# Kernel optimization log

Hardware: AMD Instinct MI355X
Metric: run time of the kernel (lower is better)

## Reference

```python
import jax, jax.numpy as jnp
import numpy as np

B, T, D, H = 4, 2048, 1152, 8
HD = D // H          # 144
ROT = HD             # full rotary
SCALE = HD ** -0.5


def _rotate_half(x):
    # x: [..., ROT]
    x1, x2 = x[..., : ROT // 2], x[..., ROT // 2 :]
    return jnp.concatenate([-x2, x1], axis=-1)


def _apply_rotary(q, k, cos, sin):
    # q,k: [B,H,T,HD]; cos,sin: [T,ROT] broadcast over B,H
    q_rot, q_pass = q[..., :ROT], q[..., ROT:]
    k_rot, k_pass = k[..., :ROT], k[..., ROT:]
    q = jnp.concatenate([q_rot * cos + _rotate_half(q_rot) * sin, q_pass], axis=-1)
    k = jnp.concatenate([k_rot * cos + _rotate_half(k_rot) * sin, k_pass], axis=-1)
    return q, k


def setup_inputs() -> dict:
    key = jax.random.key(0)
    ks = jax.random.split(key, 7)
    init = 1.0 / np.sqrt(D)  # keep activations well-scaled
    return {
        "x": jax.random.normal(ks[0], (B, T, D), dtype=jnp.float32),
        "cos": jax.random.uniform(ks[1], (T, ROT), dtype=jnp.float32),
        "sin": jax.random.uniform(ks[2], (T, ROT), dtype=jnp.float32),
        "Wq": jax.random.normal(ks[3], (D, D), dtype=jnp.float32) * init,
        "Wk": jax.random.normal(ks[4], (D, D), dtype=jnp.float32) * init,
        "Wv": jax.random.normal(ks[5], (D, D), dtype=jnp.float32) * init,
        "Wo": jax.random.normal(ks[6], (D, D), dtype=jnp.float32) * init,
    }


def reference(x, cos, sin, Wq, Wk, Wv, Wo):
    # nn.Linear(bias=False): y = x @ W.T
    def proj(W):
        y = jnp.einsum("btd,ed->bte", x, W)
        return y.reshape(B, T, H, HD).transpose(0, 2, 1, 3)  # [B,H,T,HD]

    q, k, v = proj(Wq), proj(Wk), proj(Wv)
    q, k = _apply_rotary(q, k, cos, sin)
    scores = jnp.einsum("bhqd,bhkd->bhqk", q, k) * SCALE
    attn = jax.nn.softmax(scores, axis=-1)
    o = jnp.einsum("bhqk,bhkd->bhqd", attn, v)
    o = o.transpose(0, 2, 1, 3).reshape(B, T, D)
    return jnp.einsum("btd,ed->bte", o, Wo)
```

## Files before the change

kernel.cpp:

```cpp
#include <hip/hip_runtime.h>
#include <cstdint>
#include <cstddef>

typedef __bf16 bf16;
typedef bf16 bf16x8 __attribute__((ext_vector_type(8)));
typedef bf16 bf16x4 __attribute__((ext_vector_type(4)));
typedef bf16 bf16x2 __attribute__((ext_vector_type(2)));
typedef float f32x4 __attribute__((ext_vector_type(4)));
typedef float f32x16 __attribute__((ext_vector_type(16)));
typedef uint32_t u32x2 __attribute__((ext_vector_type(2)));
typedef uint32_t u32x4 __attribute__((ext_vector_type(4)));

#define DEVI __device__ __forceinline__

#define CB 4
#define CT 2048
#define CD 1152
#define CH 8
#define CHD 144
#define CBT 8192
#define LOG2E 1.44269504f

DEVI void gload_lds16(const void* g, void* l) {
  __builtin_amdgcn_global_load_lds(
      (const __attribute__((address_space(1))) void*)g,
      (__attribute__((address_space(3))) void*)l, 16, 0, 0);
}

DEVI f32x4 mfma16(bf16x8 a, bf16x8 b, f32x4 c) {
  return __builtin_amdgcn_mfma_f32_16x16x32_bf16(a, b, c, 0, 0, 0);
}
DEVI f32x16 mfma32(bf16x8 a, bf16x8 b, f32x16 c) {
  return __builtin_amdgcn_mfma_f32_32x32x16_bf16(a, b, c, 0, 0, 0);
}

DEVI uint32_t cvtpk(float lo, float hi) {
  uint32_t r;
  asm("v_cvt_pk_bf16_f32 %0, %1, %2" : "=v"(r) : "v"(lo), "v"(hi));
  return r;
}

DEVI f32x16 zero16() {
  f32x16 z;
#pragma unroll
  for (int i = 0; i < 16; ++i) z[i] = 0.f;
  return z;
}

__global__ __launch_bounds__(256) void k_cast(const float* __restrict__ in,
                                              bf16* __restrict__ out, int n8) {
  int i = blockIdx.x * 256 + threadIdx.x;
  if (i >= n8) return;
  const float4* p = (const float4*)in + (size_t)i * 2;
  float4 a = p[0], b = p[1];
  bf16x8 o;
  o[0] = (bf16)a.x; o[1] = (bf16)a.y; o[2] = (bf16)a.z; o[3] = (bf16)a.w;
  o[4] = (bf16)b.x; o[5] = (bf16)b.y; o[6] = (bf16)b.z; o[7] = (bf16)b.w;
  ((bf16x8*)out)[i] = o;
}

__global__ __launch_bounds__(256) void k_cast4(
    const float* __restrict__ a, const float* __restrict__ b,
    const float* __restrict__ c, const float* __restrict__ d,
    bf16* __restrict__ oa, bf16* __restrict__ ob,
    bf16* __restrict__ oc, bf16* __restrict__ od, int n8) {
  int w = blockIdx.y;
  const float* in = (w == 0) ? a : (w == 1) ? b : (w == 2) ? c : d;
  bf16* out = (w == 0) ? oa : (w == 1) ? ob : (w == 2) ? oc : od;
  int i = blockIdx.x * 256 + threadIdx.x;
  if (i >= n8) return;
  const float4* p = (const float4*)in + (size_t)i * 2;
  float4 x = p[0], y = p[1];
  bf16x8 o;
  o[0] = (bf16)x.x; o[1] = (bf16)x.y; o[2] = (bf16)x.z; o[3] = (bf16)x.w;
  o[4] = (bf16)y.x; o[5] = (bf16)y.y; o[6] = (bf16)y.z; o[7] = (bf16)y.w;
  ((bf16x8*)out)[i] = o;
}

template <bool BF16_OUT>
DEVI void gemm_body(const bf16* __restrict__ A, const bf16* __restrict__ W,
                    void* __restrict__ Cout, int M, int N, int K,
                    int bm0, int bn0) {
  __shared__ __align__(16) bf16 As[128 * 40];
  __shared__ __align__(16) bf16 Bs[128 * 40];
  const int tid = threadIdx.x;
  const int lane = tid & 63, wid = tid >> 6;
  const int l15 = lane & 15, g = lane >> 4;
  const int wm = wid >> 1, wn = wid & 1;

  f32x4 acc[4][4];
  for (int mi = 0; mi < 4; ++mi)
    for (int ni = 0; ni < 4; ++ni) {
      acc[mi][ni][0] = 0.f; acc[mi][ni][1] = 0.f;
      acc[mi][ni][2] = 0.f; acc[mi][ni][3] = 0.f;
    }

  const int nk = K >> 5;
  for (int kt = 0; kt < nk; ++kt) {
    const int k0 = kt << 5;
    for (int c = 0; c < 3; ++c) {
      int li = tid + (c << 8);
      if (li < 640) {
        int e0 = li << 3;
        int row = e0 / 40, col = e0 % 40;
        if (col >= 32) col = 24;
        gload_lds16(&A[(size_t)(bm0 + row) * K + k0 + col], As + (size_t)(li & ~63) * 8);
        gload_lds16(&W[(size_t)(bn0 + row) * K + k0 + col], Bs + (size_t)(li & ~63) * 8);
      }
    }
    __syncthreads();

    bf16x8 af[4], bfr[4];
    for (int mi = 0; mi < 4; ++mi)
      af[mi] = *(const bf16x8*)&As[(wm * 64 + mi * 16 + l15) * 40 + g * 8];
    for (int ni = 0; ni < 4; ++ni)
      bfr[ni] = *(const bf16x8*)&Bs[(wn * 64 + ni * 16 + l15) * 40 + g * 8];
    __builtin_amdgcn_s_setprio(1);
    for (int mi = 0; mi < 4; ++mi)
      for (int ni = 0; ni < 4; ++ni)
        acc[mi][ni] = mfma16(af[mi], bfr[ni], acc[mi][ni]);
    __builtin_amdgcn_s_setprio(0);
    __syncthreads();
  }

  for (int mi = 0; mi < 4; ++mi)
    for (int ni = 0; ni < 4; ++ni)
      for (int r = 0; r < 4; ++r) {
        int rowg = bm0 + wm * 64 + mi * 16 + g * 4 + r;
        int colg = bn0 + wn * 64 + ni * 16 + l15;
        float v = acc[mi][ni][r];
        if (BF16_OUT)
          ((bf16*)Cout)[(size_t)rowg * N + colg] = (bf16)v;
        else
          ((float*)Cout)[(size_t)rowg * N + colg] = v;
      }
}

__global__ __launch_bounds__(256) void k_gemm_qkv(
    const bf16* __restrict__ A, const bf16* __restrict__ Wq,
    const bf16* __restrict__ Wk, const bf16* __restrict__ Wv,
    bf16* __restrict__ q, bf16* __restrict__ k, bf16* __restrict__ v) {
  const int nx = gridDim.x, ny = gridDim.y;
  const int nwg = nx * ny * gridDim.z;
  const int orig = (blockIdx.z * ny + blockIdx.y) * nx + blockIdx.x;
  const int logical = (orig & 7) * (nwg >> 3) + (orig >> 3);
  const int lx = logical % nx;
  const int rest = logical / nx;
  const int ly = rest % ny, lz = rest / ny;
  const bf16* W = (lz == 0) ? Wq : (lz == 1) ? Wk : Wv;
  bf16* out = (lz == 0) ? q : (lz == 1) ? k : v;
  gemm_body<true>(A, W, out, CBT, CD, CD, ly * 128, lx * 128);
}

__global__ __launch_bounds__(256) void k_gemm_out(
    const bf16* __restrict__ A, const bf16* __restrict__ W, float* __restrict__ out) {
  const int nx = gridDim.x, ny = gridDim.y;
  const int nwg = nx * ny;
  const int orig = blockIdx.y * nx + blockIdx.x;
  const int logical = (orig & 7) * (nwg >> 3) + (orig >> 3);
  const int lx = logical % nx, ly = logical / nx;
  gemm_body<false>(A, W, out, CBT, CD, CD, ly * 128, lx * 128);
}

__global__ __launch_bounds__(256) void k_rotary(bf16* __restrict__ q, bf16* __restrict__ k,
                                                const float* __restrict__ cosb,
                                                const float* __restrict__ sinb) {
  const int bt = blockIdx.x;
  const int t = bt & (CT - 1);
  const size_t rowoff = (size_t)bt * CD;
  const float* cr = cosb + (size_t)t * CHD;
  const float* sr = sinb + (size_t)t * CHD;
  for (int i = threadIdx.x; i < 288; i += 256) {
    int tensor = i / 144;
    int rem = i - tensor * 144;
    int h = rem / 18, jg = rem % 18;
    int j = jg * 4;
    float scl = tensor ? 1.0f : 0.08333333333f;
    bf16* base = (tensor ? k : q) + rowoff + h * CHD;
    bf16x4 a = *(bf16x4*)&base[j];
    bf16x4 b2 = *(bf16x4*)&base[j + 72];
    f32x4 c1 = *(const f32x4*)&cr[j];
    f32x4 s1 = *(const f32x4*)&sr[j];
    f32x4 c2 = *(const f32x4*)&cr[j + 72];
    f32x4 s2 = *(const f32x4*)&sr[j + 72];
    bf16x4 o1, o2;
    for (int r = 0; r < 4; ++r) {
      float av = (float)a[r], bv = (float)b2[r];
      o1[r] = (bf16)((av * c1[r] - bv * s1[r]) * scl);
      o2[r] = (bf16)((bv * c2[r] + av * s2[r]) * scl);
    }
    *(bf16x4*)&base[j] = o1;
    *(bf16x4*)&base[j + 72] = o2;
  }
}

__global__ __launch_bounds__(256) void k_vtrans(const bf16* __restrict__ v, bf16* __restrict__ vT) {
  __shared__ bf16 tile[64][152];
  const int bh = blockIdx.y;
  const int b = bh >> 3, h = bh & 7;
  const int t0 = blockIdx.x * 64;
  for (int i8 = threadIdx.x; i8 < 64 * 18; i8 += 256) {
    int r = i8 / 18, c8 = i8 % 18;
    *(bf16x8*)&tile[r][c8 * 8] =
        *(const bf16x8*)&v[((size_t)(b * CT + t0 + r)) * CD + h * CHD + c8 * 8];
  }
  __syncthreads();
  for (int o = threadIdx.x; o < CHD * 64; o += 256) {
    int hd = o / 64, j = o & 63;
    vT[((size_t)(bh * CHD + hd)) * CT + t0 + j] = tile[j][hd];
  }
}

DEVI void build_pfrag(const f32x16& s, float m, float& ps, bf16x8& f0, bf16x8& f1) {
  uint32_t pk[8];
#pragma unroll
  for (int a = 0; a < 8; ++a) {
    float p0 = exp2f((s[2 * a] - m) * LOG2E);
    float p1 = exp2f((s[2 * a + 1] - m) * LOG2E);
    ps += p0 + p1;
    pk[a] = cvtpk(p0, p1);
  }
  u32x2 r02 = __builtin_amdgcn_permlane32_swap(pk[0], pk[2], false, false);
  u32x2 r13 = __builtin_amdgcn_permlane32_swap(pk[1], pk[3], false, false);
  u32x2 r46 = __builtin_amdgcn_permlane32_swap(pk[4], pk[6], false, false);
  u32x2 r57 = __builtin_amdgcn_permlane32_swap(pk[5], pk[7], false, false);
  u32x4 w0 = {r02[0], r13[0], r02[1], r13[1]};
  u32x4 w1 = {r46[0], r57[0], r46[1], r57[1]};
  f0 = __builtin_bit_cast(bf16x8, w0);
  f1 = __builtin_bit_cast(bf16x8, w1);
}

__global__ __launch_bounds__(512, 2) void k_attn(const bf16* __restrict__ qg,
                                                 const bf16* __restrict__ kg,
                                                 const bf16* __restrict__ vT,
                                                 bf16* __restrict__ og) {
  const int lin = blockIdx.x;
  const int xcd = lin & 7, idx = lin >> 3;
  const int bh = ((idx & 3) << 3) | xcd;
  const int qx = idx >> 2;
  const int b = bh >> 3, h = bh & 7;
  const int q0 = qx << 8;
  const int tid = threadIdx.x, lane = tid & 63, wq = tid >> 6;
  const int l31 = lane & 31, hi = lane >> 5;
  const int hi16 = hi * 16;
  const int kxor = (l31 & 7) << 4;

  constexpr int KBUF = 64 * 192;
  constexpr int VBUF = 160 * 64;
  __shared__ __align__(16) bf16 Ks[2 * KBUF];
  __shared__ __align__(16) bf16 Vs[2 * VBUF];

  bf16x8 qf[9];
  {
    const bf16* qbase = qg + (size_t)(b * CT + q0 + wq * 32 + l31) * CD + h * CHD + hi * 8;
#pragma unroll
    for (int ks = 0; ks < 9; ++ks) qf[ks] = *(const bf16x8*)&qbase[ks * 16];
  }

  const bf16* ksrc[3];
  const bf16* vsrc[3];
  int kldo[3], vldo[3];
#pragma unroll
  for (int it = 0; it < 3; ++it) {
    int c = tid + it * 512;
    int krow = c / 24, kj = c - krow * 24;
    int kcol = (kj * 16) ^ ((krow & 7) << 4);
    if (kcol >= 288) kcol = 0;
    ksrc[it] = kg + (size_t)(b * CT + krow) * CD + h * CHD + (kcol >> 1);
    kldo[it] = ((tid & ~63) + it * 512) * 8;
    int vr = c >> 3, vj = c & 7;
    int vcol = (vj * 16) ^ ((vr & 7) << 4);
    if (vr > 143) vr = 143;
    vsrc[it] = vT + (size_t)(bh * CHD + vr) * CT + (vcol >> 1);
    vldo[it] = ((tid & ~63) + it * 512) * 8;
  }
  const bool vok2 = (tid < 128);

  if (tid < 256) {
    u32x4 z = {0u, 0u, 0u, 0u};
    int bsel = tid >> 7, off = tid & 127;
    *(u32x4*)(Vs + bsel * VBUF + 144 * 64 + off * 8) = z;
  }

  {
    bf16* Kc = Ks;
    bf16* Vc = Vs;
#pragma unroll
    for (int it = 0; it < 3; ++it) gload_lds16(ksrc[it], Kc + kldo[it]);
#pragma unroll
    for (int it = 0; it < 2; ++it) gload_lds16(vsrc[it], Vc + vldo[it]);
    if (vok2) gload_lds16(vsrc[2], Vc + vldo[2]);
  }
  __syncthreads();

  f32x16 oacc[5];
#pragma unroll
  for (int t = 0; t < 5; ++t) oacc[t] = zero16();
  float mrow = -__builtin_inff();
  float lsum = 0.f;

  int cur = 0;
  for (int t = 0; t < 32; ++t) {
    bf16* Kc = Ks + cur * KBUF;
    bf16* Vc = Vs + cur * VBUF;

    if (t < 31) {
      bf16* Kn = Ks + (cur ^ 1) * KBUF;
      bf16* Vn = Vs + (cur ^ 1) * VBUF;
      const int kvn = (t + 1) << 6;
#pragma unroll
      for (int it = 0; it < 3; ++it) gload_lds16(ksrc[it] + (size_t)kvn * CD, Kn + kldo[it]);
#pragma unroll
      for (int it = 0; it < 2; ++it) gload_lds16(vsrc[it] + kvn, Vn + vldo[it]);
      if (vok2) gload_lds16(vsrc[2] + kvn, Vn + vldo[2]);
    }
    __builtin_amdgcn_sched_barrier(0);

    const char* kr0 = (const char*)Kc + (size_t)l31 * 384;
    const char* kr1 = kr0 + 32 * 384;
    f32x16 s0 = zero16(), s1 = zero16();
    __builtin_amdgcn_s_setprio(1);
#pragma unroll
    for (int ks = 0; ks < 9; ++ks) {
      int off = (ks * 32 + hi16) ^ kxor;
      s0 = mfma32(*(const bf16x8*)(kr0 + off), qf[ks], s0);
      s1 = mfma32(*(const bf16x8*)(kr1 + off), qf[ks], s1);
    }
    __builtin_amdgcn_s_setprio(0);

    float mt = s0[0];
#pragma unroll
    for (int i = 1; i < 16; ++i) mt = fmaxf(mt, s0[i]);
#pragma unroll
    for (int i = 0; i < 16; ++i) mt = fmaxf(mt, s1[i]);
    mt = fmaxf(mt, __shfl_xor(mt, 32));

    if (mt > mrow + 5.5452f) {
      float alpha = exp2f((mrow - mt) * LOG2E);
      lsum *= alpha;
#pragma unroll
      for (int u = 0; u < 5; ++u) oacc[u] = oacc[u] * alpha;
      mrow = mt;
    }

    float ps = 0.f;
    bf16x8 pf0, pf1, pf2, pf3;
    build_pfrag(s0, mrow, ps, pf0, pf1);
    build_pfrag(s1, mrow, ps, pf2, pf3);
    ps += __shfl_xor(ps, 32);
    lsum += ps;

    __builtin_amdgcn_s_setprio(1);
#pragma unroll
    for (int u = 0; u < 5; ++u) {
      const char* vrow = (const char*)Vc + (size_t)(u * 32 + l31) * 128;
      oacc[u] = mfma32(*(const bf16x8*)(vrow + ((0 * 32 + hi16) ^ kxor)), pf0, oacc[u]);
      oacc[u] = mfma32(*(const bf16x8*)(vrow + ((1 * 32 + hi16) ^ kxor)), pf1, oacc[u]);
      oacc[u] = mfma32(*(const bf16x8*)(vrow + ((2 * 32 + hi16) ^ kxor)), pf2, oacc[u]);
      oacc[u] = mfma32(*(const bf16x8*)(vrow + ((3 * 32 + hi16) ^ kxor)), pf3, oacc[u]);
    }
    __builtin_amdgcn_s_setprio(0);

    __syncthreads();
    cur ^= 1;
  }

  float inv = 1.0f / lsum;
  bf16* ob = og + (size_t)(b * CT + q0 + wq * 32 + l31) * CD + h * CHD;
#pragma unroll
  for (int u = 0; u < 5; ++u) {
#pragma unroll
    for (int pr = 0; pr < 8; ++pr) {
      if (u == 4 && pr >= 4) continue;
      int hd = u * 32 + ((2 * pr) & 3) + 8 * (pr >> 1) + 4 * hi;
      bf16x2 w;
      w[0] = (bf16)(oacc[u][2 * pr] * inv);
      w[1] = (bf16)(oacc[u][2 * pr + 1] * inv);
      *(bf16x2*)&ob[hd] = w;
    }
  }
}

extern "C" void kernel_launch(void* const* d_in, const int* in_sizes, int n_in,
                              void* d_out, int out_size, void* d_ws, size_t ws_size,
                              hipStream_t stream) {
  const float* x = (const float*)d_in[0];
  const float* cosb = (const float*)d_in[1];
  const float* sinb = (const float*)d_in[2];
  const float* Wq = (const float*)d_in[3];
  const float* Wk = (const float*)d_in[4];
  const float* Wv = (const float*)d_in[5];
  const float* Wo = (const float*)d_in[6];

  char* ws = (char*)d_ws;
  bf16* xb   = (bf16*)(ws + 0);
  bf16* wqb  = (bf16*)(ws + 18874368);
  bf16* wkb  = (bf16*)(ws + 21528576);
  bf16* wvb  = (bf16*)(ws + 24182784);
  bf16* wob  = (bf16*)(ws + 26836992);
  bf16* qlin = (bf16*)(ws + 29491200);
  bf16* klin = (bf16*)(ws + 48365568);
  bf16* vlin = (bf16*)(ws + 67239936);
  bf16* vT   = (bf16*)(ws + 86114304);

  k_cast<<<4608, 256, 0, stream>>>(x, xb, CBT * CD / 8);
  k_cast4<<<dim3(648, 4), 256, 0, stream>>>(Wq, Wk, Wv, Wo, wqb, wkb, wvb, wob,
                                            CD * CD / 8);

  k_gemm_qkv<<<dim3(CD / 128, CBT / 128, 3), 256, 0, stream>>>(xb, wqb, wkb, wvb,
                                                               qlin, klin, vlin);
  k_rotary<<<CB * CT, 256, 0, stream>>>(qlin, klin, cosb, sinb);
  k_vtrans<<<dim3(CT / 64, CB * CH), 256, 0, stream>>>(vlin, vT);
  k_attn<<<256, 512, 0, stream>>>(qlin, klin, vT, xb);
  k_gemm_out<<<dim3(CD / 128, CBT / 128), 256, 0, stream>>>(xb, wob, (float*)d_out);
}
```

Baseline: 275.9 us.

## Software-pipeline attention: overlap next QK^T with current softmax and PV

Restructures the attention loop so the QK^T scores for tile t are computed while tile t-1's softmax and PV MMAs run. V gets a triple-buffered LDS ring to match the lagged consumption. The log2(e) factor is folded into the Q pre-scale in the rotary kernel, which drops a multiply per exponent. The rescale threshold is raised and the row max uses a tree reduction. This costs more LDS and registers (two sets of score accumulators), which may limit occupancy at 2 blocks per CU.

```diff
diff --git a/kernel.cpp b/kernel.cpp
--- a/kernel.cpp
+++ b/kernel.cpp
@@ -19,7 +19,6 @@
 #define CH 8
 #define CHD 144
 #define CBT 8192
-#define LOG2E 1.44269504f
 
 DEVI void gload_lds16(const void* g, void* l) {
   __builtin_amdgcn_global_load_lds(
@@ -175,7 +174,7 @@
     int rem = i - tensor * 144;
     int h = rem / 18, jg = rem % 18;
     int j = jg * 4;
-    float scl = tensor ? 1.0f : 0.08333333333f;
+    float scl = tensor ? 1.0f : 0.120224587f;
     bf16* base = (tensor ? k : q) + rowoff + h * CHD;
     bf16x4 a = *(bf16x4*)&base[j];
     bf16x4 b2 = *(bf16x4*)&base[j + 72];
@@ -215,8 +214,8 @@
   uint32_t pk[8];
 #pragma unroll
   for (int a = 0; a < 8; ++a) {
-    float p0 = exp2f((s[2 * a] - m) * LOG2E);
-    float p1 = exp2f((s[2 * a + 1] - m) * LOG2E);
+    float p0 = exp2f(s[2 * a] - m);
+    float p1 = exp2f(s[2 * a + 1] - m);
     ps += p0 + p1;
     pk[a] = cvtpk(p0, p1);
   }
@@ -228,6 +227,19 @@
   u32x4 w1 = {r46[0], r57[0], r46[1], r57[1]};
   f0 = __builtin_bit_cast(bf16x8, w0);
   f1 = __builtin_bit_cast(bf16x8, w1);
+}
+
+DEVI float max32(const f32x16& s0, const f32x16& s1) {
+  float q0 = fmaxf(fmaxf(s0[0], s0[1]), fmaxf(s0[2], s0[3]));
+  float q1 = fmaxf(fmaxf(s0[4], s0[5]), fmaxf(s0[6], s0[7]));
+  float q2 = fmaxf(fmaxf(s0[8], s0[9]), fmaxf(s0[10], s0[11]));
+  float q3 = fmaxf(fmaxf(s0[12], s0[13]), fmaxf(s0[14], s0[15]));
+  float q4 = fmaxf(fmaxf(s1[0], s1[1]), fmaxf(s1[2], s1[3]));
+  float q5 = fmaxf(fmaxf(s1[4], s1[5]), fmaxf(s1[6], s1[7]));
+  float q6 = fmaxf(fmaxf(s1[8], s1[9]), fmaxf(s1[10], s1[11]));
+  float q7 = fmaxf(fmaxf(s1[12], s1[13]), fmaxf(s1[14], s1[15]));
+  return fmaxf(fmaxf(fmaxf(q0, q1), fmaxf(q2, q3)),
+               fmaxf(fmaxf(q4, q5), fmaxf(q6, q7)));
 }
 
 __global__ __launch_bounds__(512, 2) void k_attn(const bf16* __restrict__ qg,
@@ -248,7 +260,7 @@
   constexpr int KBUF = 64 * 192;
   constexpr int VBUF = 160 * 64;
   __shared__ __align__(16) bf16 Ks[2 * KBUF];
-  __shared__ __align__(16) bf16 Vs[2 * VBUF];
+  __shared__ __align__(16) bf16 Vs[3 * VBUF];
 
   bf16x8 qf[9];
   {
@@ -276,80 +288,77 @@
   }
   const bool vok2 = (tid < 128);
 
-  if (tid < 256) {
+  if (tid < 384) {
     u32x4 z = {0u, 0u, 0u, 0u};
     int bsel = tid >> 7, off = tid & 127;
     *(u32x4*)(Vs + bsel * VBUF + 144 * 64 + off * 8) = z;
   }
 
+#define STAGE_TILE(kv, kb, vb)                                              \
+  do {                                                                      \
+    bf16* Kn = Ks + (kb) * KBUF;                                            \
+    bf16* Vn = Vs + (vb) * VBUF;                                            \
+    _Pragma("unroll") for (int it = 0; it < 3; ++it)                        \
+        gload_lds16(ksrc[it] + (size_t)(kv) * CD, Kn + kldo[it]);           \
+    _Pragma("unroll") for (int it = 0; it < 2; ++it)                        \
+        gload_lds16(vsrc[it] + (kv), Vn + vldo[it]);                        \
+    if (vok2) gload_lds16(vsrc[2] + (kv), Vn + vldo[2]);                    \
+  } while (0)
+
+  STAGE_TILE(0, 0, 0);
+  __syncthreads();
+
+  f32x16 oacc[5];
+#pragma unroll
+  for (int u = 0; u < 5; ++u) oacc[u] = zero16();
+  float lsum = 0.f;
+  float m;
+  f32x16 sp0, sp1;
+
   {
-    bf16* Kc = Ks;
-    bf16* Vc = Vs;
-#pragma unroll
-    for (int it = 0; it < 3; ++it) gload_lds16(ksrc[it], Kc + kldo[it]);
-#pragma unroll
-    for (int it = 0; it < 2; ++it) gload_lds16(vsrc[it], Vc + vldo[it]);
-    if (vok2) gload_lds16(vsrc[2], Vc + vldo[2]);
-  }
-  __syncthreads();
-
-  f32x16 oacc[5];
-#pragma unroll
-  for (int t = 0; t < 5; ++t) oacc[t] = zero16();
-  float mrow = -__builtin_inff();
-  float lsum = 0.f;
-
-  int cur = 0;
-  for (int t = 0; t < 32; ++t) {
-    bf16* Kc = Ks + cur * KBUF;
-    bf16* Vc = Vs + cur * VBUF;
-
-    if (t < 31) {
-      bf16* Kn = Ks + (cur ^ 1) * KBUF;
-      bf16* Vn = Vs + (cur ^ 1) * VBUF;
-      const int kvn = (t + 1) << 6;
-#pragma unroll
-      for (int it = 0; it < 3; ++it) gload_lds16(ksrc[it] + (size_t)kvn * CD, Kn + kldo[it]);
-#pragma unroll
-      for (int it = 0; it < 2; ++it) gload_lds16(vsrc[it] + kvn, Vn + vldo[it]);
-      if (vok2) gload_lds16(vsrc[2] + kvn, Vn + vldo[2]);
-    }
+    STAGE_TILE(64, 1, 1);
     __builtin_amdgcn_sched_barrier(0);
-
-    const char* kr0 = (const char*)Kc + (size_t)l31 * 384;
+    const char* kr0 = (const char*)Ks + (size_t)l31 * 384;
     const char* kr1 = kr0 + 32 * 384;
-    f32x16 s0 = zero16(), s1 = zero16();
+    sp0 = zero16(); sp1 = zero16();
     __builtin_amdgcn_s_setprio(1);
 #pragma unroll
     for (int ks = 0; ks < 9; ++ks) {
       int off = (ks * 32 + hi16) ^ kxor;
-      s0 = mfma32(*(const bf16x8*)(kr0 + off), qf[ks], s0);
-      s1 = mfma32(*(const bf16x8*)(kr1 + off), qf[ks], s1);
+      sp0 = mfma32(*(const bf16x8*)(kr0 + off), qf[ks], sp0);
+      sp1 = mfma32(*(const bf16x8*)(kr1 + off), qf[ks], sp1);
     }
     __builtin_amdgcn_s_setprio(0);
-
-    float mt = s0[0];
-#pragma unroll
-    for (int i = 1; i < 16; ++i) mt = fmaxf(mt, s0[i]);
-#pragma unroll
-    for (int i = 0; i < 16; ++i) mt = fmaxf(mt, s1[i]);
+    float mt = max32(sp0, sp1);
     mt = fmaxf(mt, __shfl_xor(mt, 32));
-
-    if (mt > mrow + 5.5452f) {
-      float alpha = exp2f((mrow - mt) * LOG2E);
-      lsum *= alpha;
-#pragma unroll
-      for (int u = 0; u < 5; ++u) oacc[u] = oacc[u] * alpha;
-      mrow = mt;
-    }
+    m = mt;
+    __syncthreads();
+  }
+
+  for (int t = 1; t < 32; ++t) {
+    if (t < 31) STAGE_TILE((t + 1) << 6, (t + 1) & 1, (t + 1) % 3);
+    __builtin_amdgcn_sched_barrier(0);
+
+    const char* kr0 = (const char*)(Ks + (t & 1) * KBUF) + (size_t)l31 * 384;
+    const char* kr1 = kr0 + 32 * 384;
+    f32x16 sn0 = zero16(), sn1 = zero16();
+    __builtin_amdgcn_s_setprio(1);
+#pragma unroll
+    for (int ks = 0; ks < 9; ++ks) {
+      int off = (ks * 32 + hi16) ^ kxor;
+      sn0 = mfma32(*(const bf16x8*)(kr0 + off), qf[ks], sn0);
+      sn1 = mfma32(*(const bf16x8*)(kr1 + off), qf[ks], sn1);
+    }
+    __builtin_amdgcn_s_setprio(0);
 
     float ps = 0.f;
     bf16x8 pf0, pf1, pf2, pf3;
-    build_pfrag(s0, mrow, ps, pf0, pf1);
-    build_pfrag(s1, mrow, ps, pf2, pf3);
+    build_pfrag(sp0, m, ps, pf0, pf1);
+    build_pfrag(sp1, m, ps, pf2, pf3);
     ps += __shfl_xor(ps, 32);
     lsum += ps;
 
+    const bf16* Vc = Vs + ((t - 1) % 3) * VBUF;
     __builtin_amdgcn_s_setprio(1);
 #pragma unroll
     for (int u = 0; u < 5; ++u) {
@@ -361,9 +370,37 @@
     }
     __builtin_amdgcn_s_setprio(0);
 
+    float mt = max32(sn0, sn1);
+    mt = fmaxf(mt, __shfl_xor(mt, 32));
+    if (mt > m + 8.0f) {
+      float alpha = exp2f(m - mt);
+      lsum *= alpha;
+#pragma unroll
+      for (int u = 0; u < 5; ++u) oacc[u] = oacc[u] * alpha;
+      m = mt;
+    }
+    sp0 = sn0; sp1 = sn1;
     __syncthreads();
-    cur ^= 1;
-  }
+  }
+
+  {
+    float ps = 0.f;
+    bf16x8 pf0, pf1, pf2, pf3;
+    build_pfrag(sp0, m, ps, pf0, pf1);
+    build_pfrag(sp1, m, ps, pf2, pf3);
+    ps += __shfl_xor(ps, 32);
+    lsum += ps;
+    const bf16* Vc = Vs + (31 % 3) * VBUF;
+#pragma unroll
+    for (int u = 0; u < 5; ++u) {
+      const char* vrow = (const char*)Vc + (size_t)(u * 32 + l31) * 128;
+      oacc[u] = mfma32(*(const bf16x8*)(vrow + ((0 * 32 + hi16) ^ kxor)), pf0, oacc[u]);
+      oacc[u] = mfma32(*(const bf16x8*)(vrow + ((1 * 32 + hi16) ^ kxor)), pf1, oacc[u]);
+      oacc[u] = mfma32(*(const bf16x8*)(vrow + ((2 * 32 + hi16) ^ kxor)), pf2, oacc[u]);
+      oacc[u] = mfma32(*(const bf16x8*)(vrow + ((3 * 32 + hi16) ^ kxor)), pf3, oacc[u]);
+    }
+  }
+#undef STAGE_TILE
 
   float inv = 1.0f / lsum;
   bf16* ob = og + (size_t)(b * CT + q0 + wq * 32 + l31) * CD + h * CHD;
```

Result: slower. 281.8 us (+2.1%).

## Double-buffer GEMM LDS tiles and fold log2e into the Q scale

Applied to the files above, without the earlier changes.

The projection GEMM now keeps two LDS buffers per operand and issues the next K-slice's global-to-LDS loads before computing on the current slice. This hides load latency behind the MFMAs at the cost of twice the LDS. Separately, log2(e) is folded into the rotary Q scale so the softmax exp2 calls drop a multiply. The row-max reduction is rewritten as a tree, and the lazy-rescale threshold is retuned to the new base-2 units.

```diff
diff --git a/kernel.cpp b/kernel.cpp
--- a/kernel.cpp
+++ b/kernel.cpp
@@ -19,7 +19,6 @@
 #define CH 8
 #define CHD 144
 #define CBT 8192
-#define LOG2E 1.44269504f
 
 DEVI void gload_lds16(const void* g, void* l) {
   __builtin_amdgcn_global_load_lds(
@@ -81,12 +80,40 @@
 DEVI void gemm_body(const bf16* __restrict__ A, const bf16* __restrict__ W,
                     void* __restrict__ Cout, int M, int N, int K,
                     int bm0, int bn0) {
-  __shared__ __align__(16) bf16 As[128 * 40];
-  __shared__ __align__(16) bf16 Bs[128 * 40];
+  constexpr int TBUF = 128 * 40;
+  __shared__ __align__(16) bf16 As[2 * TBUF];
+  __shared__ __align__(16) bf16 Bs[2 * TBUF];
   const int tid = threadIdx.x;
   const int lane = tid & 63, wid = tid >> 6;
   const int l15 = lane & 15, g = lane >> 4;
   const int wm = wid >> 1, wn = wid & 1;
+
+  const bf16* asrc[3];
+  const bf16* wsrc[3];
+  int ldo[3];
+  bool on[3];
+#pragma unroll
+  for (int c = 0; c < 3; ++c) {
+    int li = tid + (c << 8);
+    on[c] = (li < 640);
+    int li2 = on[c] ? li : 0;
+    int e0 = li2 << 3;
+    int row = e0 / 40, col = e0 % 40;
+    if (col >= 32) col = 24;
+    asrc[c] = &A[(size_t)(bm0 + row) * K + col];
+    wsrc[c] = &W[(size_t)(bn0 + row) * K + col];
+    ldo[c] = (li2 & ~63) * 8;
+  }
+
+#define G_STAGE(k0, buf)                                                     \
+  do {                                                                       \
+    bf16* Ad = As + (buf)*TBUF;                                              \
+    bf16* Bd = Bs + (buf)*TBUF;                                              \
+    _Pragma("unroll") for (int c = 0; c < 3; ++c) if (on[c]) {               \
+      gload_lds16(asrc[c] + (k0), Ad + ldo[c]);                              \
+      gload_lds16(wsrc[c] + (k0), Bd + ldo[c]);                              \
+    }                                                                        \
+  } while (0)
 
   f32x4 acc[4][4];
   for (int mi = 0; mi < 4; ++mi)
@@ -96,32 +123,30 @@
     }
 
   const int nk = K >> 5;
+  G_STAGE(0, 0);
+  __syncthreads();
+
+  int cur = 0;
   for (int kt = 0; kt < nk; ++kt) {
-    const int k0 = kt << 5;
-    for (int c = 0; c < 3; ++c) {
-      int li = tid + (c << 8);
-      if (li < 640) {
-        int e0 = li << 3;
-        int row = e0 / 40, col = e0 % 40;
-        if (col >= 32) col = 24;
-        gload_lds16(&A[(size_t)(bm0 + row) * K + k0 + col], As + (size_t)(li & ~63) * 8);
-        gload_lds16(&W[(size_t)(bn0 + row) * K + k0 + col], Bs + (size_t)(li & ~63) * 8);
-      }
-    }
-    __syncthreads();
-
+    if (kt + 1 < nk) G_STAGE((kt + 1) << 5, cur ^ 1);
+    __builtin_amdgcn_sched_barrier(0);
+
+    const bf16* Ac = As + cur * TBUF;
+    const bf16* Bc = Bs + cur * TBUF;
     bf16x8 af[4], bfr[4];
     for (int mi = 0; mi < 4; ++mi)
-      af[mi] = *(const bf16x8*)&As[(wm * 64 + mi * 16 + l15) * 40 + g * 8];
+      af[mi] = *(const bf16x8*)&Ac[(wm * 64 + mi * 16 + l15) * 40 + g * 8];
     for (int ni = 0; ni < 4; ++ni)
-      bfr[ni] = *(const bf16x8*)&Bs[(wn * 64 + ni * 16 + l15) * 40 + g * 8];
+      bfr[ni] = *(const bf16x8*)&Bc[(wn * 64 + ni * 16 + l15) * 40 + g * 8];
     __builtin_amdgcn_s_setprio(1);
     for (int mi = 0; mi < 4; ++mi)
       for (int ni = 0; ni < 4; ++ni)
         acc[mi][ni] = mfma16(af[mi], bfr[ni], acc[mi][ni]);
     __builtin_amdgcn_s_setprio(0);
     __syncthreads();
-  }
+    cur ^= 1;
+  }
+#undef G_STAGE
 
   for (int mi = 0; mi < 4; ++mi)
     for (int ni = 0; ni < 4; ++ni)
@@ -175,7 +200,7 @@
     int rem = i - tensor * 144;
     int h = rem / 18, jg = rem % 18;
     int j = jg * 4;
-    float scl = tensor ? 1.0f : 0.08333333333f;
+    float scl = tensor ? 1.0f : 0.120224587f;
     bf16* base = (tensor ? k : q) + rowoff + h * CHD;
     bf16x4 a = *(bf16x4*)&base[j];
     bf16x4 b2 = *(bf16x4*)&base[j + 72];
@@ -215,8 +240,8 @@
   uint32_t pk[8];
 #pragma unroll
   for (int a = 0; a < 8; ++a) {
-    float p0 = exp2f((s[2 * a] - m) * LOG2E);
-    float p1 = exp2f((s[2 * a + 1] - m) * LOG2E);
+    float p0 = exp2f(s[2 * a] - m);
+    float p1 = exp2f(s[2 * a + 1] - m);
     ps += p0 + p1;
     pk[a] = cvtpk(p0, p1);
   }
@@ -228,6 +253,19 @@
   u32x4 w1 = {r46[0], r57[0], r46[1], r57[1]};
   f0 = __builtin_bit_cast(bf16x8, w0);
   f1 = __builtin_bit_cast(bf16x8, w1);
+}
+
+DEVI float max32(const f32x16& s0, const f32x16& s1) {
+  float q0 = fmaxf(fmaxf(s0[0], s0[1]), fmaxf(s0[2], s0[3]));
+  float q1 = fmaxf(fmaxf(s0[4], s0[5]), fmaxf(s0[6], s0[7]));
+  float q2 = fmaxf(fmaxf(s0[8], s0[9]), fmaxf(s0[10], s0[11]));
+  float q3 = fmaxf(fmaxf(s0[12], s0[13]), fmaxf(s0[14], s0[15]));
+  float q4 = fmaxf(fmaxf(s1[0], s1[1]), fmaxf(s1[2], s1[3]));
+  float q5 = fmaxf(fmaxf(s1[4], s1[5]), fmaxf(s1[6], s1[7]));
+  float q6 = fmaxf(fmaxf(s1[8], s1[9]), fmaxf(s1[10], s1[11]));
+  float q7 = fmaxf(fmaxf(s1[12], s1[13]), fmaxf(s1[14], s1[15]));
+  return fmaxf(fmaxf(fmaxf(q0, q1), fmaxf(q2, q3)),
+               fmaxf(fmaxf(q4, q5), fmaxf(q6, q7)));
 }
 
 __global__ __launch_bounds__(512, 2) void k_attn(const bf16* __restrict__ qg,
@@ -282,20 +320,23 @@
     *(u32x4*)(Vs + bsel * VBUF + 144 * 64 + off * 8) = z;
   }
 
-  {
-    bf16* Kc = Ks;
-    bf16* Vc = Vs;
-#pragma unroll
-    for (int it = 0; it < 3; ++it) gload_lds16(ksrc[it], Kc + kldo[it]);
-#pragma unroll
-    for (int it = 0; it < 2; ++it) gload_lds16(vsrc[it], Vc + vldo[it]);
-    if (vok2) gload_lds16(vsrc[2], Vc + vldo[2]);
-  }
+#define STAGE_TILE(kv, buf)                                                 \
+  do {                                                                      \
+    bf16* Kn = Ks + (buf)*KBUF;                                             \
+    bf16* Vn = Vs + (buf)*VBUF;                                             \
+    _Pragma("unroll") for (int it = 0; it < 3; ++it)                        \
+        gload_lds16(ksrc[it] + (size_t)(kv)*CD, Kn + kldo[it]);             \
+    _Pragma("unroll") for (int it = 0; it < 2; ++it)                        \
+        gload_lds16(vsrc[it] + (kv), Vn + vldo[it]);                        \
+    if (vok2) gload_lds16(vsrc[2] + (kv), Vn + vldo[2]);                    \
+  } while (0)
+
+  STAGE_TILE(0, 0);
   __syncthreads();
 
   f32x16 oacc[5];
 #pragma unroll
-  for (int t = 0; t < 5; ++t) oacc[t] = zero16();
+  for (int u = 0; u < 5; ++u) oacc[u] = zero16();
   float mrow = -__builtin_inff();
   float lsum = 0.f;
 
@@ -304,16 +345,7 @@
     bf16* Kc = Ks + cur * KBUF;
     bf16* Vc = Vs + cur * VBUF;
 
-    if (t < 31) {
-      bf16* Kn = Ks + (cur ^ 1) * KBUF;
-      bf16* Vn = Vs + (cur ^ 1) * VBUF;
-      const int kvn = (t + 1) << 6;
-#pragma unroll
-      for (int it = 0; it < 3; ++it) gload_lds16(ksrc[it] + (size_t)kvn * CD, Kn + kldo[it]);
-#pragma unroll
-      for (int it = 0; it < 2; ++it) gload_lds16(vsrc[it] + kvn, Vn + vldo[it]);
-      if (vok2) gload_lds16(vsrc[2] + kvn, Vn + vldo[2]);
-    }
+    if (t < 31) STAGE_TILE((t + 1) << 6, cur ^ 1);
     __builtin_amdgcn_sched_barrier(0);
 
     const char* kr0 = (const char*)Kc + (size_t)l31 * 384;
@@ -328,15 +360,11 @@
     }
     __builtin_amdgcn_s_setprio(0);
 
-    float mt = s0[0];
-#pragma unroll
-    for (int i = 1; i < 16; ++i) mt = fmaxf(mt, s0[i]);
-#pragma unroll
-    for (int i = 0; i < 16; ++i) mt = fmaxf(mt, s1[i]);
+    float mt = max32(s0, s1);
     mt = fmaxf(mt, __shfl_xor(mt, 32));
 
-    if (mt > mrow + 5.5452f) {
-      float alpha = exp2f((mrow - mt) * LOG2E);
+    if (mt > mrow + 8.0f) {
+      float alpha = exp2f(mrow - mt);
       lsum *= alpha;
 #pragma unroll
       for (int u = 0; u < 5; ++u) oacc[u] = oacc[u] * alpha;
@@ -364,6 +392,7 @@
     __syncthreads();
     cur ^= 1;
   }
+#undef STAGE_TILE
 
   float inv = 1.0f / lsum;
   bf16* ob = og + (size_t)(b * CT + q0 + wq * 32 + l31) * CD + h * CHD;
```

New measurement: 263.7 us. -4.4%, faster.
